# Performance work log

Measured on AMD Instinct MI355X. Metric: run time of the kernel, lower is better.

Reference implementation:

```python
import jax, jax.numpy as jnp
import numpy as np

N = 131072  # nodes
E = 4096    # edges (unused by forward)
MID = 32    # multiplicity of irreps_mid = 32x0e + 32x1o
NF = 128    # multiplicity of node_feat_irreps = 128x0e + 128x1o
INV_SQRT3 = 0.5773502691896258          # |w3j(1,1,0)| = |w3j(0,1,1)| = 1/sqrt(3)
PW_QQ_S = (1.0 / 2048.0) ** 0.5         # path weight: alpha = dim(0e)/ (32*32 + 32*32)
PW_QQ_V = (3.0 / 2048.0) ** 0.5         # path weight: alpha = dim(1o)/ (32*32 + 32*32)
PW_DOWN = (1.0 / 8192.0) ** 0.5         # path weight: alpha = dim(0e)/ (32*128 + 32*128)


def setup_inputs() -> dict:
    key = jax.random.key(0)
    ks = jax.random.split(key, 20)
    inp = {
        "node_feats": jax.random.normal(ks[0], (N, NF + 3 * NF), jnp.float32),
        "charges_0": jax.random.normal(ks[1], (N, 4), jnp.float32),
        "charges_induced": jax.random.normal(ks[2], (N, 4), jnp.float32),
        "edge_feats": jax.random.normal(ks[3], (E, 8), jnp.float32),
        "edge_attrs": jax.random.normal(ks[4], (E, 9), jnp.float32),
        "field_feats": jax.random.normal(ks[5], (N, 4), jnp.float32),
        "edge_index": jax.random.randint(ks[6], (2, E), 0, N, dtype=jnp.int32),
        "batch": jnp.sort(jax.random.randint(ks[7], (N,), 0, 64, dtype=jnp.int32)),
        # o3.Linear(1x0e+1x1o -> 32x0e+32x1o) params (fan_in = 1 per path -> norm 1)
        "Wa_s": jax.random.normal(ks[8], (1, MID), jnp.float32),
        "Wa_v": jax.random.normal(ks[9], (1, MID), jnp.float32),
        "b_a": jnp.zeros((MID,), jnp.float32),
        "Wb_s": jax.random.normal(ks[10], (1, MID), jnp.float32),
        "Wb_v": jax.random.normal(ks[11], (1, MID), jnp.float32),
        "b_b": jnp.zeros((MID,), jnp.float32),
        # FullyConnectedTensorProduct(mid, mid -> mid) uvw weights, one per CG path
        "W_ss": jax.random.normal(ks[12], (MID, MID, MID), jnp.float32),  # 0e x 0e -> 0e
        "W_vv": jax.random.normal(ks[13], (MID, MID, MID), jnp.float32),  # 1o x 1o -> 0e
        "W_sv": jax.random.normal(ks[14], (MID, MID, MID), jnp.float32),  # 0e x 1o -> 1o
        "W_vs": jax.random.normal(ks[15], (MID, MID, MID), jnp.float32),  # 1o x 0e -> 1o
        # FullyConnectedTensorProduct(mid, node_feats -> 1x0e) uvw weights
        "Wd_s": jax.random.normal(ks[16], (MID, NF), jnp.float32),        # 0e x 0e -> 0e
        "Wd_v": jax.random.normal(ks[17], (MID, NF), jnp.float32),        # 1o x 1o -> 0e
    }
    return inp


def reference(node_feats, charges_0, charges_induced, edge_feats, edge_attrs,
              field_feats, edge_index, batch,
              Wa_s, Wa_v, b_a, Wb_s, Wb_v, b_b,
              W_ss, W_vv, W_sv, W_vs, Wd_s, Wd_v):
    # split irreps blocks
    s0, v0 = charges_0[:, :1], charges_0[:, 1:4]            # [N,1], [N,3]
    si, vi = charges_induced[:, :1], charges_induced[:, 1:4]
    nf_s = node_feats[:, :NF]                               # [N,128]
    nf_v = node_feats[:, NF:].reshape(-1, NF, 3)            # [N,128,3]

    # charges = linear_qa(charges_induced) + linear_qb(charges_0)  (bias only on 0e)
    s = si @ Wa_s + b_a + s0 @ Wb_s + b_b                   # [N,32]
    v = (jnp.einsum('nui,uw->nwi', vi[:, None, :], Wa_v)
         + jnp.einsum('nui,uw->nwi', v0[:, None, :], Wb_v))  # [N,32,3]

    # qq = FullyConnectedTensorProduct(charges, charges) -> 32x0e + 32x1o
    qs = PW_QQ_S * (jnp.einsum('nu,nv,uvw->nw', s, s, W_ss)
                    + INV_SQRT3 * jnp.einsum('nui,nvi,uvw->nw', v, v, W_vv))      # [N,32]
    qv = (PW_QQ_V * INV_SQRT3) * (jnp.einsum('nu,nvi,uvw->nwi', s, v, W_sv)
                                  + jnp.einsum('nui,nv,uvw->nwi', v, s, W_vs))    # [N,32,3]

    # energy = FullyConnectedTensorProduct(qq, node_feats) -> 1x0e, then squeeze
    energy = PW_DOWN * (jnp.einsum('nu,nv,uv->n', qs, nf_s, Wd_s)
                        + INV_SQRT3 * jnp.einsum('nui,nvi,uv->n', qv, nf_v, Wd_v))  # [N]
    return energy
```

## Files before the change

kernel.cpp:

```cpp
#include <hip/hip_runtime.h>


#define NNODES 131072
#define TBLK 256
#define NODES_PER_PASS 8
#define PASSES 8
#define NPB (NODES_PER_PASS * PASSES)

__global__ void precompute_coeff(
    const float* __restrict__ Wa_s, const float* __restrict__ Wa_v,
    const float* __restrict__ b_a,  const float* __restrict__ Wb_s,
    const float* __restrict__ Wb_v, const float* __restrict__ b_b,
    const float* __restrict__ W_ss, const float* __restrict__ W_vv,
    const float* __restrict__ W_sv, const float* __restrict__ W_vs,
    float* __restrict__ partial)
{
  __shared__ float As[32], Bs[32], Cc[32], Avv[32], Bvv[32];
  __shared__ float red[8][480];
  const int t = threadIdx.x;
  if (t < 32) {
    As[t] = Wa_s[t]; Bs[t] = Wb_s[t]; Cc[t] = b_a[t] + b_b[t];
    Avv[t] = Wa_v[t]; Bvv[t] = Wb_v[t];
  }
  __syncthreads();
  const int w = t & 31;
  const int grp = t >> 5;
  const int chunk = blockIdx.x * 8 + grp;
  float acc[15];
  #pragma unroll
  for (int k = 0; k < 15; ++k) acc[k] = 0.f;
  #pragma unroll
  for (int j = 0; j < 4; ++j) {
    const int p = chunk * 4 + j;
    const int u = p >> 5, v = p & 31;
    const float wss = W_ss[p * 32 + w];
    const float wvv = W_vv[p * 32 + w];
    const float wsv = W_sv[p * 32 + w];
    const float wvs = W_vs[p * 32 + w];
    const float au = As[u], bu = Bs[u], cu = Cc[u], pu = Avv[u], qu = Bvv[u];
    const float av = As[v], bv = Bs[v], cv = Cc[v], pv = Avv[v], qv = Bvv[v];
    acc[0]  = fmaf(au * av, wss, acc[0]);
    acc[1]  = fmaf(au * bv + bu * av, wss, acc[1]);
    acc[2]  = fmaf(bu * bv, wss, acc[2]);
    acc[3]  = fmaf(au * cv + cu * av, wss, acc[3]);
    acc[4]  = fmaf(bu * cv + cu * bv, wss, acc[4]);
    acc[5]  = fmaf(cu * cv, wss, acc[5]);
    acc[6]  = fmaf(pu * pv, wvv, acc[6]);
    acc[7]  = fmaf(pu * qv + qu * pv, wvv, acc[7]);
    acc[8]  = fmaf(qu * qv, wvv, acc[8]);
    acc[9]  = fmaf(au * pv, wsv, fmaf(pu * av, wvs, acc[9]));
    acc[10] = fmaf(au * qv, wsv, fmaf(qu * av, wvs, acc[10]));
    acc[11] = fmaf(bu * pv, wsv, fmaf(pu * bv, wvs, acc[11]));
    acc[12] = fmaf(bu * qv, wsv, fmaf(qu * bv, wvs, acc[12]));
    acc[13] = fmaf(cu * pv, wsv, fmaf(pu * cv, wvs, acc[13]));
    acc[14] = fmaf(cu * qv, wsv, fmaf(qu * cv, wvs, acc[14]));
  }
  #pragma unroll
  for (int k = 0; k < 15; ++k) red[grp][k * 32 + w] = acc[k];
  __syncthreads();
  for (int kk = grp; kk < 15; kk += 8) {
    float s = 0.f;
    #pragma unroll
    for (int b = 0; b < 8; ++b) s += red[b][kk * 32 + w];
    partial[blockIdx.x * 480 + kk * 32 + w] = s;
  }
}

__global__ void precompute_M(
    const float* __restrict__ Wd_s, const float* __restrict__ Wd_v,
    const float* __restrict__ partial,
    float* __restrict__ Ms, float* __restrict__ Mv)
{
  __shared__ float cf[480];
  const int t = threadIdx.x;
  if (t < 480) {
    float s = 0.f;
    for (int b = 0; b < 32; ++b) s += partial[b * 480 + t];
    cf[t] = s;
  }
  __syncthreads();
  if (t < 128) {
    const int f = t;
    float as[9], av[6];
    #pragma unroll
    for (int k = 0; k < 9; ++k) as[k] = 0.f;
    #pragma unroll
    for (int k = 0; k < 6; ++k) av[k] = 0.f;
    for (int w = 0; w < 32; ++w) {
      const float wds = Wd_s[w * 128 + f];
      const float wdv = Wd_v[w * 128 + f];
      #pragma unroll
      for (int k = 0; k < 9; ++k) as[k] = fmaf(cf[k * 32 + w], wds, as[k]);
      #pragma unroll
      for (int k = 0; k < 6; ++k) av[k] = fmaf(cf[(9 + k) * 32 + w], wdv, av[k]);
    }
    const float sP = 1.0f / 4096.0f;
    const float sQ = 0.57735026918962576451f / 4096.0f;
    #pragma unroll
    for (int k = 0; k < 6; ++k) Ms[f * 16 + k] = as[k] * sP;
    #pragma unroll
    for (int k = 0; k < 3; ++k) Ms[f * 16 + 6 + k] = as[6 + k] * sQ;
    #pragma unroll
    for (int k = 0; k < 6; ++k) Mv[f * 8 + k] = av[k] * sQ;
  }
}

__global__ __launch_bounds__(TBLK) void energy_main(
    const float* __restrict__ nf,
    const float* __restrict__ ch0,
    const float* __restrict__ chi,
    const float* __restrict__ Ms,
    const float* __restrict__ Mv,
    float* __restrict__ out)
{
  const int t    = threadIdx.x;
  const int s32  = t & 31;
  const int gidx = t >> 5;

  float ms[4][9];
  float mv[4][6];
  {
    const float4* Ms4 = reinterpret_cast<const float4*>(Ms);
    const float4* Mv4 = reinterpret_cast<const float4*>(Mv);
    #pragma unroll
    for (int fl = 0; fl < 4; ++fl) {
      const int f = 4 * s32 + fl;
      const float4 a = Ms4[f * 4 + 0];
      const float4 b = Ms4[f * 4 + 1];
      const float4 c = Ms4[f * 4 + 2];
      ms[fl][0] = a.x; ms[fl][1] = a.y; ms[fl][2] = a.z; ms[fl][3] = a.w;
      ms[fl][4] = b.x; ms[fl][5] = b.y; ms[fl][6] = b.z; ms[fl][7] = b.w;
      ms[fl][8] = c.x;
      const float4 u = Mv4[f * 2 + 0];
      const float4 v = Mv4[f * 2 + 1];
      mv[fl][0] = u.x; mv[fl][1] = u.y; mv[fl][2] = u.z; mv[fl][3] = u.w;
      mv[fl][4] = v.x; mv[fl][5] = v.y;
    }
  }

  const float4* nf4 = reinterpret_cast<const float4*>(nf);
  const float4* c04 = reinterpret_cast<const float4*>(ch0);
  const float4* ci4 = reinterpret_cast<const float4*>(chi);

  const int node0 = blockIdx.x * NPB;

  #pragma unroll 2
  for (int p = 0; p < PASSES; ++p) {
    const int node  = node0 + p * NODES_PER_PASS + gidx;
    const size_t rb = (size_t)node * 128;

    const float4 cc0 = c04[node];
    const float4 cci = ci4[node];
    const float4 xs  = nf4[rb + s32];
    const float4 xv0 = nf4[rb + 32 + 3 * s32 + 0];
    const float4 xv1 = nf4[rb + 32 + 3 * s32 + 1];
    const float4 xv2 = nf4[rb + 32 + 3 * s32 + 2];

    const float alpha = cci.x, g0 = cci.y, g1 = cci.z, g2 = cci.w;
    const float beta  = cc0.x, d0 = cc0.y, d1 = cc0.z, d2 = cc0.w;
    const float m0 = alpha * alpha, m1 = alpha * beta, m2 = beta * beta;
    const float m6 = fmaf(g0, g0, fmaf(g1, g1, g2 * g2));
    const float m7 = fmaf(g0, d0, fmaf(g1, d1, g2 * d2));
    const float m8 = fmaf(d0, d0, fmaf(d1, d1, d2 * d2));

    float e = 0.f;

    const float xse[4] = {xs.x, xs.y, xs.z, xs.w};
    #pragma unroll
    for (int fl = 0; fl < 4; ++fl) {
      float r = ms[fl][5];
      r = fmaf(m0,    ms[fl][0], r);
      r = fmaf(m1,    ms[fl][1], r);
      r = fmaf(m2,    ms[fl][2], r);
      r = fmaf(alpha, ms[fl][3], r);
      r = fmaf(beta,  ms[fl][4], r);
      r = fmaf(m6,    ms[fl][6], r);
      r = fmaf(m7,    ms[fl][7], r);
      r = fmaf(m8,    ms[fl][8], r);
      e = fmaf(xse[fl], r, e);
    }

    const float xve[12] = {xv0.x, xv0.y, xv0.z, xv0.w,
                           xv1.x, xv1.y, xv1.z, xv1.w,
                           xv2.x, xv2.y, xv2.z, xv2.w};
    const float gg[3] = {g0, g1, g2};
    const float dd[3] = {d0, d1, d2};
    float P = 0.f, Q = 0.f;
    #pragma unroll
    for (int q = 0; q < 12; ++q) {
      const int i = q % 3;
      P = fmaf(gg[i], xve[q], P);
      Q = fmaf(dd[i], xve[q], Q);
      if (i == 2) {
        const int fl = q / 3;
        const float wP = fmaf(alpha, mv[fl][0], fmaf(beta, mv[fl][2], mv[fl][4]));
        const float wQ = fmaf(alpha, mv[fl][1], fmaf(beta, mv[fl][3], mv[fl][5]));
        e = fmaf(P, wP, fmaf(Q, wQ, e));
        P = 0.f; Q = 0.f;
      }
    }

    e += __shfl_xor(e, 1);
    e += __shfl_xor(e, 2);
    e += __shfl_xor(e, 4);
    e += __shfl_xor(e, 8);
    e += __shfl_xor(e, 16);
    if (s32 == 0) out[node] = e;
  }
}

extern "C" void kernel_launch(void* const* d_in, const int* in_sizes, int n_in,
                              void* d_out, int out_size, void* d_ws, size_t ws_size,
                              hipStream_t stream)
{
  const float* node_feats      = (const float*)d_in[0];
  const float* charges_0       = (const float*)d_in[1];
  const float* charges_induced = (const float*)d_in[2];
  const float* Wa_s = (const float*)d_in[8];
  const float* Wa_v = (const float*)d_in[9];
  const float* b_a  = (const float*)d_in[10];
  const float* Wb_s = (const float*)d_in[11];
  const float* Wb_v = (const float*)d_in[12];
  const float* b_b  = (const float*)d_in[13];
  const float* W_ss = (const float*)d_in[14];
  const float* W_vv = (const float*)d_in[15];
  const float* W_sv = (const float*)d_in[16];
  const float* W_vs = (const float*)d_in[17];
  const float* Wd_s = (const float*)d_in[18];
  const float* Wd_v = (const float*)d_in[19];

  float* ws      = (float*)d_ws;
  float* Ms      = ws;
  float* Mv      = ws + 2048;
  float* partial = ws + 3072;

  precompute_coeff<<<32, 256, 0, stream>>>(Wa_s, Wa_v, b_a, Wb_s, Wb_v, b_b,
                                           W_ss, W_vv, W_sv, W_vs, partial);
  precompute_M<<<1, 512, 0, stream>>>(Wd_s, Wd_v, partial, Ms, Mv);
  energy_main<<<NNODES / NPB, TBLK, 0, stream>>>(node_feats, charges_0,
                                                 charges_induced, Ms, Mv,
                                                 (float*)d_out);
}
```

Before: 412.8 us.

## Map one node per wave64 with float2 loads, software prefetch, nontemporal access

Reassigns work so a full 64-lane wave handles one node using 8-byte loads, instead of 32 lanes each issuing 16-byte loads. Next-pass loads are issued explicitly before the current pass's math, and all streaming loads and the output store use nontemporal hints. Occupancy is raised via launch_bounds with a minimum block count, and an extra shuffle stage finishes the 64-lane reduction. The kernel is bandwidth bound, so the gain depends on whether more outstanding requests outweigh the narrower per-lane accesses.

```diff
diff --git a/kernel.cpp b/kernel.cpp
--- a/kernel.cpp
+++ b/kernel.cpp
@@ -3,9 +3,12 @@
 
 #define NNODES 131072
 #define TBLK 256
-#define NODES_PER_PASS 8
-#define PASSES 8
-#define NPB (NODES_PER_PASS * PASSES)
+#define WAVES_PER_BLK 4
+#define PASSES 16
+#define NPB (WAVES_PER_BLK * PASSES)
+
+typedef float f32x2 __attribute__((ext_vector_type(2)));
+typedef float f32x4 __attribute__((ext_vector_type(4)));
 
 __global__ void precompute_coeff(
     const float* __restrict__ Wa_s, const float* __restrict__ Wa_v,
@@ -105,7 +108,7 @@
   }
 }
 
-__global__ __launch_bounds__(TBLK) void energy_main(
+__global__ __launch_bounds__(TBLK, 5) void energy_main(
     const float* __restrict__ nf,
     const float* __restrict__ ch0,
     const float* __restrict__ chi,
@@ -113,18 +116,19 @@
     const float* __restrict__ Mv,
     float* __restrict__ out)
 {
-  const int t    = threadIdx.x;
-  const int s32  = t & 31;
-  const int gidx = t >> 5;
-
-  float ms[4][9];
-  float mv[4][6];
+  static_assert(NPB * (NNODES / NPB) == NNODES, "grid covers all nodes");
+  const int t  = threadIdx.x;
+  const int l  = t & 63;
+  const int wv = t >> 6;
+
+  float ms[2][9];
+  float mv[2][6];
   {
     const float4* Ms4 = reinterpret_cast<const float4*>(Ms);
     const float4* Mv4 = reinterpret_cast<const float4*>(Mv);
     #pragma unroll
-    for (int fl = 0; fl < 4; ++fl) {
-      const int f = 4 * s32 + fl;
+    for (int fl = 0; fl < 2; ++fl) {
+      const int f = 2 * l + fl;
       const float4 a = Ms4[f * 4 + 0];
       const float4 b = Ms4[f * 4 + 1];
       const float4 c = Ms4[f * 4 + 2];
@@ -138,26 +142,43 @@
     }
   }
 
-  const float4* nf4 = reinterpret_cast<const float4*>(nf);
-  const float4* c04 = reinterpret_cast<const float4*>(ch0);
-  const float4* ci4 = reinterpret_cast<const float4*>(chi);
+  const f32x2* nf2 = reinterpret_cast<const f32x2*>(nf);
+  const f32x4* c04 = reinterpret_cast<const f32x4*>(ch0);
+  const f32x4* ci4 = reinterpret_cast<const f32x4*>(chi);
 
   const int node0 = blockIdx.x * NPB;
-
-  #pragma unroll 2
+  const int voff  = 64 + 3 * l;
+
+  f32x2 pxs, pv0, pv1, pv2;
+  f32x4 pc0, pci;
+
+#define LOADSET(pp) do {                                             \
+    const int nn_    = node0 + (pp) * WAVES_PER_BLK + wv;            \
+    const size_t rb2 = (size_t)nn_ * 256;                            \
+    pc0 = __builtin_nontemporal_load(c04 + nn_);                     \
+    pci = __builtin_nontemporal_load(ci4 + nn_);                     \
+    pxs = __builtin_nontemporal_load(nf2 + rb2 + l);                 \
+    pv0 = __builtin_nontemporal_load(nf2 + rb2 + voff + 0);          \
+    pv1 = __builtin_nontemporal_load(nf2 + rb2 + voff + 1);          \
+    pv2 = __builtin_nontemporal_load(nf2 + rb2 + voff + 2);          \
+  } while (0)
+
+  LOADSET(0);
+
+  #pragma unroll
   for (int p = 0; p < PASSES; ++p) {
-    const int node  = node0 + p * NODES_PER_PASS + gidx;
-    const size_t rb = (size_t)node * 128;
-
-    const float4 cc0 = c04[node];
-    const float4 cci = ci4[node];
-    const float4 xs  = nf4[rb + s32];
-    const float4 xv0 = nf4[rb + 32 + 3 * s32 + 0];
-    const float4 xv1 = nf4[rb + 32 + 3 * s32 + 1];
-    const float4 xv2 = nf4[rb + 32 + 3 * s32 + 2];
-
-    const float alpha = cci.x, g0 = cci.y, g1 = cci.z, g2 = cci.w;
-    const float beta  = cc0.x, d0 = cc0.y, d1 = cc0.z, d2 = cc0.w;
+    const f32x2 xs  = pxs;
+    const f32x2 xv0 = pv0;
+    const f32x2 xv1 = pv1;
+    const f32x2 xv2 = pv2;
+    const f32x4 cc0 = pc0;
+    const f32x4 cci = pci;
+    if (p + 1 < PASSES) LOADSET(p + 1);
+
+    const int node = node0 + p * WAVES_PER_BLK + wv;
+
+    const float alpha = cci[0], g0 = cci[1], g1 = cci[2], g2 = cci[3];
+    const float beta  = cc0[0], d0 = cc0[1], d1 = cc0[2], d2 = cc0[3];
     const float m0 = alpha * alpha, m1 = alpha * beta, m2 = beta * beta;
     const float m6 = fmaf(g0, g0, fmaf(g1, g1, g2 * g2));
     const float m7 = fmaf(g0, d0, fmaf(g1, d1, g2 * d2));
@@ -165,9 +186,9 @@
 
     float e = 0.f;
 
-    const float xse[4] = {xs.x, xs.y, xs.z, xs.w};
-    #pragma unroll
-    for (int fl = 0; fl < 4; ++fl) {
+    const float xse[2] = {xs[0], xs[1]};
+    #pragma unroll
+    for (int fl = 0; fl < 2; ++fl) {
       float r = ms[fl][5];
       r = fmaf(m0,    ms[fl][0], r);
       r = fmaf(m1,    ms[fl][1], r);
@@ -180,24 +201,15 @@
       e = fmaf(xse[fl], r, e);
     }
 
-    const float xve[12] = {xv0.x, xv0.y, xv0.z, xv0.w,
-                           xv1.x, xv1.y, xv1.z, xv1.w,
-                           xv2.x, xv2.y, xv2.z, xv2.w};
-    const float gg[3] = {g0, g1, g2};
-    const float dd[3] = {d0, d1, d2};
-    float P = 0.f, Q = 0.f;
-    #pragma unroll
-    for (int q = 0; q < 12; ++q) {
-      const int i = q % 3;
-      P = fmaf(gg[i], xve[q], P);
-      Q = fmaf(dd[i], xve[q], Q);
-      if (i == 2) {
-        const int fl = q / 3;
-        const float wP = fmaf(alpha, mv[fl][0], fmaf(beta, mv[fl][2], mv[fl][4]));
-        const float wQ = fmaf(alpha, mv[fl][1], fmaf(beta, mv[fl][3], mv[fl][5]));
-        e = fmaf(P, wP, fmaf(Q, wQ, e));
-        P = 0.f; Q = 0.f;
-      }
+    const float xva[2][3] = {{xv0[0], xv0[1], xv1[0]},
+                             {xv1[1], xv2[0], xv2[1]}};
+    #pragma unroll
+    for (int fl = 0; fl < 2; ++fl) {
+      const float P = fmaf(g0, xva[fl][0], fmaf(g1, xva[fl][1], g2 * xva[fl][2]));
+      const float Q = fmaf(d0, xva[fl][0], fmaf(d1, xva[fl][1], d2 * xva[fl][2]));
+      const float wP = fmaf(alpha, mv[fl][0], fmaf(beta, mv[fl][2], mv[fl][4]));
+      const float wQ = fmaf(alpha, mv[fl][1], fmaf(beta, mv[fl][3], mv[fl][5]));
+      e = fmaf(P, wP, fmaf(Q, wQ, e));
     }
 
     e += __shfl_xor(e, 1);
@@ -205,8 +217,10 @@
     e += __shfl_xor(e, 4);
     e += __shfl_xor(e, 8);
     e += __shfl_xor(e, 16);
-    if (s32 == 0) out[node] = e;
-  }
+    e += __shfl_xor(e, 32);
+    if (l == 0) __builtin_nontemporal_store(e, out + node);
+  }
+#undef LOADSET
 }
 
 extern "C" void kernel_launch(void* const* d_in, const int* in_sizes, int n_in,
```

Measured after the change: 405.5 us. No clear change (-1.8%).
